# Kernel optimization log

Hardware: AMD Instinct MI355X
Metric: run time of the kernel (lower is better)

Reference implementation:

```python
import jax, jax.numpy as jnp
import numpy as np
from jax import lax

TAU = 2.0      # LIF membrane time constant
VTH = 0.5      # spike threshold
ALPHA = 4.0    # sigmoid surrogate gradient sharpness (spikingjelly default)
EPS = 1e-5     # BatchNorm eps
HEADS = 8

@jax.custom_vjp
def _spike(x):
    return (x >= 0.0).astype(x.dtype)

def _spike_fwd(x):
    return _spike(x), x

def _spike_bwd(x, g):
    s = jax.nn.sigmoid(ALPHA * x)
    return (g * ALPHA * s * (1.0 - s),)

_spike.defvjp(_spike_fwd, _spike_bwd)

def lif(x_seq):
    # multi-step LIF, decay_input=True, hard reset to 0, detach_reset=True
    def step(v, x):
        v = v + (x - v) / TAU
        s = _spike(v - VTH)
        v = v * (1.0 - lax.stop_gradient(s))
        return v, s
    _, s_seq = lax.scan(step, jnp.zeros_like(x_seq[0]), x_seq)
    return s_seq

def bn(x, gamma, beta, mean, var):
    # inference-mode BatchNorm over channel axis 2 of [T,B,C,H,W]
    sh = (1, 1, -1, 1, 1)
    scale = gamma.reshape(sh) / jnp.sqrt(var.reshape(sh) + EPS)
    return (x - mean.reshape(sh)) * scale + beta.reshape(sh)

def conv1x1(x, w, b=None):
    y = jnp.einsum('oc,tbchw->tbohw', w, x)
    if b is not None:
        y = y + b.reshape(1, 1, -1, 1, 1)
    return y

def setup_inputs() -> dict:
    key = jax.random.key(0)
    T, B, C, H, W = 4, 8, 384, 32, 32
    ks = jax.random.split(key, 20)
    s = 1.0 / np.sqrt(C)
    d = {
        'x': jax.random.normal(ks[0], (T, B, C, H, W), jnp.float32),
        'q_w': jax.random.normal(ks[1], (C, C), jnp.float32) * s,
        'k_w': jax.random.normal(ks[2], (C, C), jnp.float32) * s,
        'v_w': jax.random.normal(ks[3], (C, C), jnp.float32) * s,
        'th_w': jax.random.normal(ks[4], (HEADS, HEADS), jnp.float32) * (1.0 / np.sqrt(HEADS)),
        'proj_w': jax.random.normal(ks[5], (C, C), jnp.float32) * s,
        'proj_b': jax.random.normal(ks[6], (C,), jnp.float32) * 0.01,
    }
    for i, p in enumerate(['q', 'k', 'v', 'proj']):
        kk = jax.random.split(ks[7 + i], 4)
        d[f'{p}_gamma'] = 1.0 + 0.1 * jax.random.normal(kk[0], (C,), jnp.float32)
        d[f'{p}_beta'] = 0.1 * jax.random.normal(kk[1], (C,), jnp.float32)
        d[f'{p}_mean'] = 0.1 * jax.random.normal(kk[2], (C,), jnp.float32)
        d[f'{p}_var'] = jax.random.uniform(kk[3], (C,), jnp.float32, 0.5, 1.5)
    return d

def reference(x, q_w, k_w, v_w, th_w, proj_w, proj_b,
              q_gamma, q_beta, q_mean, q_var,
              k_gamma, k_beta, k_mean, k_var,
              v_gamma, v_beta, v_mean, v_var,
              proj_gamma, proj_beta, proj_mean, proj_var):
    T, B, C, H, W = x.shape
    hd = C // HEADS
    N = H * W
    identity = x
    xs = lif(x)  # shortcut_lif

    def branch(w, g, be, m, va):
        return lif(bn(conv1x1(xs, w), g, be, m, va))

    def split_heads(t):  # [T,B,C,H,W] -> [T,B,heads,N,hd]
        return t.reshape(T, B, HEADS, hd, N).transpose(0, 1, 2, 4, 3)

    q = split_heads(branch(q_w, q_gamma, q_beta, q_mean, q_var))
    k = split_heads(branch(k_w, k_gamma, k_beta, k_mean, k_var))
    v = split_heads(branch(v_w, v_gamma, v_beta, v_mean, v_var))

    kv = (k * v).sum(axis=3)                      # [T,B,heads,hd]
    kv = jnp.einsum('oh,tbhd->tbod', th_w, kv)     # talking heads (Conv1d 1x1, no bias)
    kv = lif(kv)[:, :, :, None, :]                 # [T,B,heads,1,hd]

    x_att = q * kv                                 # broadcast over N
    x_att = x_att.transpose(0, 1, 2, 4, 3).reshape(T, B, C, H, W)
    out = bn(conv1x1(x_att, proj_w, proj_b), proj_gamma, proj_beta, proj_mean, proj_var)
    return out + identity
```

## Files before the change

kernel.cpp:

```cpp
#include <hip/hip_runtime.h>
#include <stdint.h>


typedef unsigned short u16;
typedef __attribute__((ext_vector_type(8))) short short8v;
typedef __attribute__((ext_vector_type(4))) float f32x4;

#define AS1 __attribute__((address_space(1)))
#define AS3 __attribute__((address_space(3)))

__device__ __forceinline__ void async16(const void* g, void* l) {
    __builtin_amdgcn_global_load_lds((const AS1 unsigned int*)g,
                                     (AS3 unsigned int*)l, 16, 0, 0);
}
__device__ __forceinline__ f32x4 mfma_bf16(short8v a, short8v b, f32x4 c) {
    return __builtin_amdgcn_mfma_f32_16x16x32_bf16(a, b, c, 0, 0, 0);
}
__device__ __forceinline__ f32x4 mfma_f16(short8v a, short8v b, f32x4 c) {
    return __builtin_amdgcn_mfma_f32_16x16x32_f16(a, b, c, 0, 0, 0);
}

__device__ __forceinline__ u16 f2bf(float f) {
    uint32_t x = __float_as_uint(f);
    return (u16)((x + 0x7FFFu + ((x >> 16) & 1u)) >> 16);
}

#define SPIKE_H ((u16)0x3C00)
#define SPIKE_B ((u16)0x3F80)

__global__ void prep_kernel(const float* __restrict__ qw, const float* __restrict__ kw,
                            const float* __restrict__ vw, const float* __restrict__ pw,
                            u16* __restrict__ Ah, u16* __restrict__ Aproj) {
    int id = blockIdx.x * 256 + threadIdx.x;
    if (id >= 1152 * 384) return;
    int m = id / 384, c = id % 384;
    int br = m / 384, o = m % 384;
    const float* W = (br == 0) ? qw : (br == 1) ? kw : vw;
    float w = W[o * 384 + c];
    union H { _Float16 h; u16 u; } u0, u1;
    u0.h = (_Float16)w;
    float r1 = w - (float)u0.h;
    u1.h = (_Float16)r1;
    u16* row = Ah + (size_t)m * 768;
    row[c] = u0.u;
    row[384 + c] = u1.u;
    if (br == 0) Aproj[o * 384 + c] = f2bf(pw[o * 384 + c]);
}

__global__ __launch_bounds__(256) void lifx_kernel(const float* __restrict__ x,
                                                   u16* __restrict__ xs) {
    __shared__ u16 Tr[64 * 72];
    int b = blockIdx.z, c0 = blockIdx.y * 64, n0 = blockIdx.x * 64;
    int tid = threadIdx.x;
    int nj = (tid & 15) * 4;
    int ci = tid >> 4;
    float v[4][4];
#pragma unroll
    for (int p = 0; p < 4; p++)
#pragma unroll
        for (int e = 0; e < 4; e++) v[p][e] = 0.0f;

    for (int t = 0; t < 4; t++) {
#pragma unroll
        for (int p = 0; p < 4; p++) {
            const float* src = x + ((size_t)((t * 8 + b) * 384 + c0 + p * 16 + ci)) * 1024 + n0 + nj;
            float4 xv = *(const float4*)src;
            float xa[4] = {xv.x, xv.y, xv.z, xv.w};
#pragma unroll
            for (int e = 0; e < 4; e++) {
                float vv = v[p][e];
                vv = __fadd_rn(vv, __fmul_rn(__fsub_rn(xa[e], vv), 0.5f));
                bool sp = (vv >= 0.5f);
                v[p][e] = sp ? 0.0f : vv;
                Tr[(nj + e) * 72 + p * 16 + ci] = sp ? SPIKE_H : (u16)0;
            }
        }
        __syncthreads();
#pragma unroll
        for (int p = 0; p < 4; p++) {
            int nr = p * 16 + (tid >> 4);
            int c4 = (tid & 15) * 4;
            *(ushort4*)(xs + ((size_t)((t * 8 + b) * 1024 + n0 + nr)) * 384 + c0 + c4) =
                *(const ushort4*)&Tr[nr * 72 + c4];
        }
        __syncthreads();
    }
}

__global__ __launch_bounds__(512, 2) void qkv_kernel(
    const u16* __restrict__ Ah, const u16* __restrict__ xs,
    u16* __restrict__ qs, u16* __restrict__ ks, u16* __restrict__ vs,
    const float* __restrict__ qg, const float* __restrict__ qb, const float* __restrict__ qm, const float* __restrict__ qv,
    const float* __restrict__ kg, const float* __restrict__ kb, const float* __restrict__ km, const float* __restrict__ kvr,
    const float* __restrict__ vg, const float* __restrict__ vb, const float* __restrict__ vm, const float* __restrict__ vvr) {
    __shared__ __align__(16) u16 As[3][8192];
    __shared__ __align__(16) u16 Bs[3][16384];
    __shared__ float bnS[128], bnM[128], bnB[128];

    const int b = blockIdx.z, mt = blockIdx.y, nt = blockIdx.x;
    const int m0 = mt * 128, n0 = nt * 64;
    const int branch = mt / 3, o0 = (mt % 3) * 128;
    const int tid = threadIdx.x, wave = tid >> 6, lane = tid & 63;
    const int l15 = lane & 15, quad = lane >> 4;
    const int wmh = wave >> 2;
    const int wn4 = wave & 3;

    const float* g_  = (branch == 0) ? qg : (branch == 1) ? kg : vg;
    const float* be_ = (branch == 0) ? qb : (branch == 1) ? kb : vb;
    const float* m_  = (branch == 0) ? qm : (branch == 1) ? km : vm;
    const float* v_  = (branch == 0) ? qv : (branch == 1) ? kvr : vvr;
    u16* dstp = (branch == 0) ? qs : (branch == 1) ? ks : vs;

    if (tid < 128) {
        int o = o0 + tid;
        bnS[tid] = g_[o] / sqrtf(v_[o] + 1e-5f);
        bnM[tid] = m_[o];
        bnB[tid] = be_[o];
    }

    const int cl = tid >> 3;
    const int cs8 = ((tid & 7) ^ (cl & 7)) * 8;
    const int dst0 = tid * 8;

    const u16* pA0 = Ah + (size_t)(m0 + cl) * 768 + cs8;
    const u16* pA1 = Ah + (size_t)(m0 + 64 + cl) * 768 + cs8;
    const int tB = (cl >> 4) & 3, nB = cl & 15;
    const u16* pB0 = xs + ((size_t)((tB * 8 + b) * 1024 + n0 +  0 + nB)) * 384 + cs8;
    const u16* pB1 = xs + ((size_t)((tB * 8 + b) * 1024 + n0 + 16 + nB)) * 384 + cs8;
    const u16* pB2 = xs + ((size_t)((tB * 8 + b) * 1024 + n0 + 32 + nB)) * 384 + cs8;
    const u16* pB3 = xs + ((size_t)((tB * 8 + b) * 1024 + n0 + 48 + nB)) * 384 + cs8;

    auto stageA = [&](int Tn, int slot) { int kk = Tn * 64;
        async16(pA0 + kk, &As[slot][dst0]);
        async16(pA1 + kk, &As[slot][4096 + dst0]); };
    auto stageB01 = [&](int Tn, int slot) { int kk = Tn * 64;
        int ck = (kk >= 384) ? kk - 384 : kk;
        async16(pB0 + ck, &Bs[slot][dst0]);
        async16(pB1 + ck, &Bs[slot][4096 + dst0]); };
    auto stageB23 = [&](int Tn, int slot) { int kk = Tn * 64;
        int ck = (kk >= 384) ? kk - 384 : kk;
        async16(pB2 + ck, &Bs[slot][8192 + dst0]);
        async16(pB3 + ck, &Bs[slot][12288 + dst0]); };

    const int ch0 = (quad ^ (l15 & 7)) * 8;
    const int ch1 = ((quad + 4) ^ (l15 & 7)) * 8;
    const int arow = (wmh * 64 + l15) * 64;
    const int bcol = (wn4 * 64 + l15) * 64;

    f32x4 acc[4][4];
#pragma unroll
    for (int i = 0; i < 4; i++)
#pragma unroll
        for (int j = 0; j < 4; j++) acc[i][j] = (f32x4){0.f, 0.f, 0.f, 0.f};

    stageA(0, 0); stageB01(0, 0); stageB23(0, 0);
    stageA(1, 1); stageB01(1, 1); stageB23(1, 1);
    asm volatile("s_waitcnt vmcnt(6)\n\ts_barrier" ::: "memory");

    short8v afA[4], bfA[4], afB[4], bfB[4];
    int r = 0, r2 = 2;
#pragma unroll 1
    for (int Tn = 0; Tn < 12; Tn++) {
#pragma unroll
        for (int i = 0; i < 4; i++) afA[i] = *(const short8v*)&As[r][arow + i * 1024 + ch0];
#pragma unroll
        for (int t = 0; t < 4; t++) bfA[t] = *(const short8v*)&Bs[r][bcol + t * 1024 + ch0];
        __builtin_amdgcn_sched_barrier(0);
#pragma unroll
        for (int i = 0; i < 4; i++) afB[i] = *(const short8v*)&As[r][arow + i * 1024 + ch1];
#pragma unroll
        for (int t = 0; t < 4; t++) bfB[t] = *(const short8v*)&Bs[r][bcol + t * 1024 + ch1];
        if (Tn < 10) { stageA(Tn + 2, r2); stageB01(Tn + 2, r2); stageB23(Tn + 2, r2); }
        __builtin_amdgcn_sched_barrier(0);
        __builtin_amdgcn_s_setprio(1);
#pragma unroll
        for (int i = 0; i < 4; i++)
#pragma unroll
            for (int t = 0; t < 4; t++) acc[i][t] = mfma_f16(afA[i], bfA[t], acc[i][t]);
        __builtin_amdgcn_s_setprio(0);
        __builtin_amdgcn_sched_barrier(0);
        __builtin_amdgcn_s_setprio(1);
#pragma unroll
        for (int i = 0; i < 4; i++)
#pragma unroll
            for (int t = 0; t < 4; t++) acc[i][t] = mfma_f16(afB[i], bfB[t], acc[i][t]);
        __builtin_amdgcn_s_setprio(0);
        if (Tn < 10)       asm volatile("s_waitcnt vmcnt(6)\n\ts_barrier" ::: "memory");
        else if (Tn == 10) asm volatile("s_waitcnt vmcnt(0)\n\ts_barrier" ::: "memory");
        r = (r == 2) ? 0 : r + 1;
        r2 = (r2 == 2) ? 0 : r2 + 1;
    }

    const int nn = n0 + wn4 * 16 + l15;
#pragma unroll
    for (int i = 0; i < 4; i++) {
        int co = wmh * 64 + i * 16 + quad * 4;
        float4 s4 = *(const float4*)&bnS[co];
        float4 m4 = *(const float4*)&bnM[co];
        float4 b4 = *(const float4*)&bnB[co];
        float sc[4] = {s4.x, s4.y, s4.z, s4.w};
        float mn[4] = {m4.x, m4.y, m4.z, m4.w};
        float bt[4] = {b4.x, b4.y, b4.z, b4.w};
        u16 sv[4][4];
#pragma unroll
        for (int e = 0; e < 4; e++) {
            float vv = 0.0f;
#pragma unroll
            for (int t = 0; t < 4; t++) {
                float a = acc[i][t][e];
                a = __fadd_rn(__fmul_rn(__fsub_rn(a, mn[e]), sc[e]), bt[e]);
                vv = __fadd_rn(vv, __fmul_rn(__fsub_rn(a, vv), 0.5f));
                bool sp = (vv >= 0.5f);
                vv = sp ? 0.0f : vv;
                sv[t][e] = sp ? SPIKE_B : (u16)0;
            }
        }
#pragma unroll
        for (int t = 0; t < 4; t++) {
            ushort4 o4;
            o4.x = sv[t][0]; o4.y = sv[t][1]; o4.z = sv[t][2]; o4.w = sv[t][3];
            *(ushort4*)(dstp + ((size_t)((t * 8 + b) * 1024 + nn)) * 384 + o0 + co) = o4;
        }
    }
}

__global__ void kvred_kernel(const u16* __restrict__ ks, const u16* __restrict__ vs,
                             float* __restrict__ r2) {
    __shared__ float red[8][384];
    int tb = blockIdx.y, nc = blockIdx.x;
    int tid = threadIdx.x;
    int rr = tid / 48, c8 = tid % 48;

    float cnt[8];
#pragma unroll
    for (int e = 0; e < 8; e++) cnt[e] = 0.0f;

    size_t base = ((size_t)(tb * 1024 + nc * 64 + rr)) * 384 + c8 * 8;
#pragma unroll 2
    for (int it = 0; it < 8; it++) {
        size_t off = base + (size_t)it * 8 * 384;
        uint4 ka = *(const uint4*)(ks + off);
        uint4 va = *(const uint4*)(vs + off);
        uint32_t w0 = ka.x & va.x, w1 = ka.y & va.y, w2 = ka.z & va.z, w3 = ka.w & va.w;
        const uint32_t S = SPIKE_B;
        if ((w0 & 0xFFFFu) == S) cnt[0] += 1.0f;
        if ((w0 >> 16) == S)     cnt[1] += 1.0f;
        if ((w1 & 0xFFFFu) == S) cnt[2] += 1.0f;
        if ((w1 >> 16) == S)     cnt[3] += 1.0f;
        if ((w2 & 0xFFFFu) == S) cnt[4] += 1.0f;
        if ((w2 >> 16) == S)     cnt[5] += 1.0f;
        if ((w3 & 0xFFFFu) == S) cnt[6] += 1.0f;
        if ((w3 >> 16) == S)     cnt[7] += 1.0f;
    }
#pragma unroll
    for (int e = 0; e < 8; e++) red[rr][c8 * 8 + e] = cnt[e];
    __syncthreads();
    float s = 0.0f;
#pragma unroll
    for (int q = 0; q < 8; q++) s += red[q][tid];
    r2[((size_t)(tb * 16 + nc)) * 384 + tid] = s;
}

__global__ void ncsum_kernel(const float* __restrict__ r2, float* __restrict__ r) {
    int id = blockIdx.x * 256 + threadIdx.x;
    if (id >= 32 * 384) return;
    int tb = id / 384, c = id % 384;
    const float* p = r2 + ((size_t)(tb * 16)) * 384 + c;
    float s = 0.0f;
#pragma unroll
    for (int nc = 0; nc < 16; nc++) s += p[nc * 384];
    r[id] = s;
}

__global__ void talking_kernel(const float* __restrict__ r, const float* __restrict__ th,
                               u16* __restrict__ kvs) {
    int id = blockIdx.x * 256 + threadIdx.x;
    if (id >= 8 * 384) return;
    int b = id / 384, c = id % 384;
    int oh = c / 48, d = c % 48;
    float v = 0.0f;
    for (int t = 0; t < 4; t++) {
        const float* rr = r + (t * 8 + b) * 384 + d;
        float s = 0.0f;
#pragma unroll
        for (int h = 0; h < 8; h++) s = __fmaf_rn(th[oh * 8 + h], rr[h * 48], s);
        v = __fadd_rn(v, __fmul_rn(__fsub_rn(s, v), 0.5f));
        bool sp = (v >= 0.5f);
        v = sp ? 0.0f : v;
        kvs[(t * 8 + b) * 384 + c] = sp ? SPIKE_B : (u16)0;
    }
}

__global__ __launch_bounds__(256, 2) void proj_kernel(
    const u16* __restrict__ Aproj, const u16* __restrict__ qs, const u16* __restrict__ kvs,
    const float* __restrict__ xin,
    const float* __restrict__ pb, const float* __restrict__ pg, const float* __restrict__ pbe,
    const float* __restrict__ pm, const float* __restrict__ pv, float* __restrict__ out) {
    __shared__ __align__(16) u16 At[2][8192];
    __shared__ __align__(16) u16 Bt[2][8192];
    __shared__ float eS[128], eM[128], eB[128], eBi[128];

    int tb = blockIdx.z, mt = blockIdx.y, nt = blockIdx.x;
    int m0 = mt * 128, n0 = nt * 128;
    int tid = threadIdx.x, wave = tid >> 6, lane = tid & 63;
    int l15 = lane & 15, quad = lane >> 4;
    int wm = (wave & 1) * 64, wn = (wave >> 1) * 64;

    const u16* Bsrc = qs + ((size_t)(tb * 1024 + n0)) * 384;
    const u16* mbase = kvs + tb * 384;

    if (tid < 128) {
        int o = m0 + tid;
        eS[tid] = pg[o] / sqrtf(pv[o] + 1e-5f);
        eM[tid] = pm[o];
        eB[tid] = pbe[o];
        eBi[tid] = pb[o];
    }

    auto stage = [&](int s) {
        int kk = s * 64;
        int buf = s & 1;
#pragma unroll
        for (int ii = 0; ii < 4; ii++) {
            int l = ii * 256 + tid;
            int row = l >> 3;
            int cs = (l & 7) ^ (row & 7);
            async16(Aproj + (size_t)(m0 + row) * 384 + kk + cs * 8, &At[buf][l * 8]);
            async16(Bsrc + (size_t)row * 384 + kk + cs * 8, &Bt[buf][l * 8]);
        }
    };

    f32x4 acc[4][4];
#pragma unroll
    for (int i = 0; i < 4; i++)
#pragma unroll
        for (int j = 0; j < 4; j++) acc[i][j] = (f32x4){0.f, 0.f, 0.f, 0.f};

    stage(0);
    __syncthreads();

#pragma unroll 1
    for (int kkb = 0; kkb < 6; kkb++) {
        int buf = kkb & 1;
        int kk = kkb * 64;
        if (kkb < 5) stage(kkb + 1);
        __builtin_amdgcn_sched_barrier(0);

        short8v msk0 = *(const short8v*)(mbase + kk + quad * 8);
        short8v msk1 = *(const short8v*)(mbase + kk + (4 + quad) * 8);
        short8v afA[4], bfA[4], afB[4], bfB[4];
#pragma unroll
        for (int i = 0; i < 4; i++) {
            int row = wm + i * 16 + l15;
            afA[i] = *(const short8v*)&At[buf][row * 64 + ((quad) ^ (row & 7)) * 8];
            afB[i] = *(const short8v*)&At[buf][row * 64 + ((4 + quad) ^ (row & 7)) * 8];
        }
#pragma unroll
        for (int j = 0; j < 4; j++) {
            int nr = wn + j * 16 + l15;
            bfA[j] = *(const short8v*)&Bt[buf][nr * 64 + ((quad) ^ (nr & 7)) * 8] & msk0;
            bfB[j] = *(const short8v*)&Bt[buf][nr * 64 + ((4 + quad) ^ (nr & 7)) * 8] & msk1;
        }
        __builtin_amdgcn_sched_barrier(0);
        __builtin_amdgcn_s_setprio(1);
#pragma unroll
        for (int i = 0; i < 4; i++)
#pragma unroll
            for (int j = 0; j < 4; j++) acc[i][j] = mfma_bf16(afA[i], bfA[j], acc[i][j]);
        __builtin_amdgcn_s_setprio(0);
        __builtin_amdgcn_sched_barrier(0);
        __builtin_amdgcn_s_setprio(1);
#pragma unroll
        for (int i = 0; i < 4; i++)
#pragma unroll
            for (int j = 0; j < 4; j++) acc[i][j] = mfma_bf16(afB[i], bfB[j], acc[i][j]);
        __builtin_amdgcn_s_setprio(0);
        if (kkb < 5) asm volatile("s_waitcnt vmcnt(0)\n\ts_barrier" ::: "memory");
    }

#pragma unroll
    for (int i = 0; i < 4; i++) {
#pragma unroll
        for (int e = 0; e < 4; e++) {
            int co = wm + i * 16 + quad * 4 + e;
            int o = m0 + co;
            float scale = eS[co], mean = eM[co], beta = eB[co], bias = eBi[co];
#pragma unroll
            for (int j = 0; j < 4; j++) {
                int n = n0 + wn + j * 16 + l15;
                size_t idx = ((size_t)tb * 384 + o) * 1024 + n;
                float y = __fadd_rn(acc[i][j][e], bias);
                y = __fadd_rn(__fmul_rn(__fsub_rn(y, mean), scale), beta);
                out[idx] = __fadd_rn(y, xin[idx]);
            }
        }
    }
}

extern "C" void kernel_launch(void* const* d_in, const int* in_sizes, int n_in,
                              void* d_out, int out_size, void* d_ws, size_t ws_size,
                              hipStream_t stream) {
    (void)in_sizes; (void)n_in; (void)out_size; (void)ws_size;
    const float* x  = (const float*)d_in[0];
    const float* qw = (const float*)d_in[1];
    const float* kw = (const float*)d_in[2];
    const float* vw = (const float*)d_in[3];
    const float* th = (const float*)d_in[4];
    const float* pw = (const float*)d_in[5];
    const float* pb = (const float*)d_in[6];
    const float* qg = (const float*)d_in[7],  *qbe = (const float*)d_in[8];
    const float* qm = (const float*)d_in[9],  *qv  = (const float*)d_in[10];
    const float* kg = (const float*)d_in[11], *kbe = (const float*)d_in[12];
    const float* km = (const float*)d_in[13], *kv_ = (const float*)d_in[14];
    const float* vg = (const float*)d_in[15], *vbe = (const float*)d_in[16];
    const float* vm = (const float*)d_in[17], *vv_ = (const float*)d_in[18];
    const float* pg = (const float*)d_in[19], *pbe = (const float*)d_in[20];
    const float* pm = (const float*)d_in[21], *pv  = (const float*)d_in[22];
    float* out = (float*)d_out;

    char* w = (char*)d_ws;
    const size_t SPIKES = (size_t)32 * 1024 * 384 * 2;
    u16* xs    = (u16*)(w);
    u16* qs    = (u16*)(w + SPIKES);
    u16* ks    = (u16*)(w + 2 * SPIKES);
    u16* vs    = (u16*)(w + 3 * SPIKES);
    u16* Ah    = (u16*)(w + 4 * SPIKES);
    u16* Aproj = (u16*)(w + 4 * SPIKES + 1769472);
    float* r2  = (float*)(w + 4 * SPIKES + 1769472 + 294912);
    float* r   = (float*)(w + 4 * SPIKES + 1769472 + 294912 + 786432);
    u16* kvs   = (u16*)(w + 4 * SPIKES + 1769472 + 294912 + 786432 + 49152);

    prep_kernel<<<1728, 256, 0, stream>>>(qw, kw, vw, pw, Ah, Aproj);
    lifx_kernel<<<dim3(16, 6, 8), 256, 0, stream>>>(x, xs);
    qkv_kernel<<<dim3(16, 9, 8), 512, 0, stream>>>(Ah, xs, qs, ks, vs,
                                                   qg, qbe, qm, qv,
                                                   kg, kbe, km, kv_,
                                                   vg, vbe, vm, vv_);
    kvred_kernel<<<dim3(16, 32), 384, 0, stream>>>(ks, vs, r2);
    ncsum_kernel<<<48, 256, 0, stream>>>(r2, r);
    talking_kernel<<<12, 256, 0, stream>>>(r, th, kvs);
    proj_kernel<<<dim3(8, 3, 32), 256, 0, stream>>>(Aproj, qs, kvs, x, pb, pg, pbe, pm, pv, out);
}
```

Baseline: 251.2 us.

## Halve qkv GEMM N-tile and K-step, using 256-thread blocks

```diff
diff --git a/kernel.cpp b/kernel.cpp
--- a/kernel.cpp
+++ b/kernel.cpp
@@ -87,23 +87,23 @@
     }
 }
 
-__global__ __launch_bounds__(512, 2) void qkv_kernel(
+__global__ __launch_bounds__(256, 2) void qkv_kernel(
     const u16* __restrict__ Ah, const u16* __restrict__ xs,
     u16* __restrict__ qs, u16* __restrict__ ks, u16* __restrict__ vs,
     const float* __restrict__ qg, const float* __restrict__ qb, const float* __restrict__ qm, const float* __restrict__ qv,
     const float* __restrict__ kg, const float* __restrict__ kb, const float* __restrict__ km, const float* __restrict__ kvr,
     const float* __restrict__ vg, const float* __restrict__ vb, const float* __restrict__ vm, const float* __restrict__ vvr) {
-    __shared__ __align__(16) u16 As[3][8192];
-    __shared__ __align__(16) u16 Bs[3][16384];
+    __shared__ __align__(16) u16 As[3][4096];
+    __shared__ __align__(16) u16 Bs[3][4096];
     __shared__ float bnS[128], bnM[128], bnB[128];
 
     const int b = blockIdx.z, mt = blockIdx.y, nt = blockIdx.x;
-    const int m0 = mt * 128, n0 = nt * 64;
+    const int m0 = mt * 128, n0 = nt * 32;
     const int branch = mt / 3, o0 = (mt % 3) * 128;
     const int tid = threadIdx.x, wave = tid >> 6, lane = tid & 63;
     const int l15 = lane & 15, quad = lane >> 4;
-    const int wmh = wave >> 2;
-    const int wn4 = wave & 3;
+    const int wm2 = wave >> 1;
+    const int wn2 = wave & 1;
 
     const float* g_  = (branch == 0) ? qg : (branch == 1) ? kg : vg;
     const float* be_ = (branch == 0) ? qb : (branch == 1) ? kb : vb;
@@ -118,34 +118,28 @@
         bnB[tid] = be_[o];
     }
 
-    const int cl = tid >> 3;
-    const int cs8 = ((tid & 7) ^ (cl & 7)) * 8;
+    const int srow = tid >> 2;
+    const int cs8 = ((tid & 3) ^ ((srow >> 1) & 3)) * 8;
     const int dst0 = tid * 8;
 
-    const u16* pA0 = Ah + (size_t)(m0 + cl) * 768 + cs8;
-    const u16* pA1 = Ah + (size_t)(m0 + 64 + cl) * 768 + cs8;
-    const int tB = (cl >> 4) & 3, nB = cl & 15;
-    const u16* pB0 = xs + ((size_t)((tB * 8 + b) * 1024 + n0 +  0 + nB)) * 384 + cs8;
+    const u16* pA0 = Ah + (size_t)(m0 + srow) * 768 + cs8;
+    const u16* pA1 = Ah + (size_t)(m0 + 64 + srow) * 768 + cs8;
+    const int tB = (srow >> 4) & 3, nB = srow & 15;
+    const u16* pB0 = xs + ((size_t)((tB * 8 + b) * 1024 + n0 + nB)) * 384 + cs8;
     const u16* pB1 = xs + ((size_t)((tB * 8 + b) * 1024 + n0 + 16 + nB)) * 384 + cs8;
-    const u16* pB2 = xs + ((size_t)((tB * 8 + b) * 1024 + n0 + 32 + nB)) * 384 + cs8;
-    const u16* pB3 = xs + ((size_t)((tB * 8 + b) * 1024 + n0 + 48 + nB)) * 384 + cs8;
-
-    auto stageA = [&](int Tn, int slot) { int kk = Tn * 64;
+
+    auto stage = [&](int Tn, int slot) {
+        int kk = Tn * 32;
+        int ck = (kk >= 384) ? kk - 384 : kk;
         async16(pA0 + kk, &As[slot][dst0]);
-        async16(pA1 + kk, &As[slot][4096 + dst0]); };
-    auto stageB01 = [&](int Tn, int slot) { int kk = Tn * 64;
-        int ck = (kk >= 384) ? kk - 384 : kk;
+        async16(pA1 + kk, &As[slot][2048 + dst0]);
         async16(pB0 + ck, &Bs[slot][dst0]);
-        async16(pB1 + ck, &Bs[slot][4096 + dst0]); };
-    auto stageB23 = [&](int Tn, int slot) { int kk = Tn * 64;
-        int ck = (kk >= 384) ? kk - 384 : kk;
-        async16(pB2 + ck, &Bs[slot][8192 + dst0]);
-        async16(pB3 + ck, &Bs[slot][12288 + dst0]); };
-
-    const int ch0 = (quad ^ (l15 & 7)) * 8;
-    const int ch1 = ((quad + 4) ^ (l15 & 7)) * 8;
-    const int arow = (wmh * 64 + l15) * 64;
-    const int bcol = (wn4 * 64 + l15) * 64;
+        async16(pB1 + ck, &Bs[slot][2048 + dst0]);
+    };
+
+    const int ch = (quad ^ ((l15 >> 1) & 3)) * 8;
+    const int arow_ = (wm2 * 64 + l15) * 32 + ch;
+    const int bcol_ = (wn2 * 64 + l15) * 32 + ch;
 
     f32x4 acc[4][4];
 #pragma unroll
@@ -153,48 +147,36 @@
 #pragma unroll
         for (int j = 0; j < 4; j++) acc[i][j] = (f32x4){0.f, 0.f, 0.f, 0.f};
 
-    stageA(0, 0); stageB01(0, 0); stageB23(0, 0);
-    stageA(1, 1); stageB01(1, 1); stageB23(1, 1);
-    asm volatile("s_waitcnt vmcnt(6)\n\ts_barrier" ::: "memory");
-
-    short8v afA[4], bfA[4], afB[4], bfB[4];
-    int r = 0, r2 = 2;
+    stage(0, 0);
+    stage(1, 1);
+    asm volatile("s_waitcnt vmcnt(4)\n\ts_barrier" ::: "memory");
+
+    int r = 0, r2v = 2;
 #pragma unroll 1
-    for (int Tn = 0; Tn < 12; Tn++) {
-#pragma unroll
-        for (int i = 0; i < 4; i++) afA[i] = *(const short8v*)&As[r][arow + i * 1024 + ch0];
-#pragma unroll
-        for (int t = 0; t < 4; t++) bfA[t] = *(const short8v*)&Bs[r][bcol + t * 1024 + ch0];
-        __builtin_amdgcn_sched_barrier(0);
-#pragma unroll
-        for (int i = 0; i < 4; i++) afB[i] = *(const short8v*)&As[r][arow + i * 1024 + ch1];
-#pragma unroll
-        for (int t = 0; t < 4; t++) bfB[t] = *(const short8v*)&Bs[r][bcol + t * 1024 + ch1];
-        if (Tn < 10) { stageA(Tn + 2, r2); stageB01(Tn + 2, r2); stageB23(Tn + 2, r2); }
+    for (int Tn = 0; Tn < 24; Tn++) {
+        short8v af[4], bf[4];
+#pragma unroll
+        for (int i = 0; i < 4; i++) af[i] = *(const short8v*)&As[r][arow_ + i * 512];
+#pragma unroll
+        for (int t = 0; t < 4; t++) bf[t] = *(const short8v*)&Bs[r][bcol_ + t * 512];
+        if (Tn < 22) stage(Tn + 2, r2v);
         __builtin_amdgcn_sched_barrier(0);
         __builtin_amdgcn_s_setprio(1);
 #pragma unroll
         for (int i = 0; i < 4; i++)
 #pragma unroll
-            for (int t = 0; t < 4; t++) acc[i][t] = mfma_f16(afA[i], bfA[t], acc[i][t]);
+            for (int t = 0; t < 4; t++) acc[i][t] = mfma_f16(af[i], bf[t], acc[i][t]);
         __builtin_amdgcn_s_setprio(0);
-        __builtin_amdgcn_sched_barrier(0);
-        __builtin_amdgcn_s_setprio(1);
-#pragma unroll
-        for (int i = 0; i < 4; i++)
-#pragma unroll
-            for (int t = 0; t < 4; t++) acc[i][t] = mfma_f16(afB[i], bfB[t], acc[i][t]);
-        __builtin_amdgcn_s_setprio(0);
-        if (Tn < 10)       asm volatile("s_waitcnt vmcnt(6)\n\ts_barrier" ::: "memory");
-        else if (Tn == 10) asm volatile("s_waitcnt vmcnt(0)\n\ts_barrier" ::: "memory");
+        if (Tn < 22)       asm volatile("s_waitcnt vmcnt(4)\n\ts_barrier" ::: "memory");
+        else if (Tn == 22) asm volatile("s_waitcnt vmcnt(0)\n\ts_barrier" ::: "memory");
         r = (r == 2) ? 0 : r + 1;
-        r2 = (r2 == 2) ? 0 : r2 + 1;
-    }
-
-    const int nn = n0 + wn4 * 16 + l15;
+        r2v = (r2v == 2) ? 0 : r2v + 1;
+    }
+
+    const int nn = n0 + wn2 * 16 + l15;
 #pragma unroll
     for (int i = 0; i < 4; i++) {
-        int co = wmh * 64 + i * 16 + quad * 4;
+        int co = wm2 * 64 + i * 16 + quad * 4;
         float4 s4 = *(const float4*)&bnS[co];
         float4 m4 = *(const float4*)&bnM[co];
         float4 b4 = *(const float4*)&bnB[co];
@@ -432,7 +414,7 @@
 
     prep_kernel<<<1728, 256, 0, stream>>>(qw, kw, vw, pw, Ah, Aproj);
     lifx_kernel<<<dim3(16, 6, 8), 256, 0, stream>>>(x, xs);
-    qkv_kernel<<<dim3(16, 9, 8), 512, 0, stream>>>(Ah, xs, qs, ks, vs,
+    qkv_kernel<<<dim3(32, 9, 8), 256, 0, stream>>>(Ah, xs, qs, ks, vs,
                                                    qg, qbe, qm, qv,
                                                    kg, kbe, km, kv_,
                                                    vg, vbe, vm, vv_);
```

After: 258.5 us. +2.9%, slower.
